# Kernel optimization log

Hardware: AMD Instinct MI355X
Metric: run time of the kernel (lower is better)

## Reference

```python
import jax, jax.numpy as jnp
import numpy as np

N_EMBD = 1024
N_HEAD = 16
HEAD = N_EMBD // N_HEAD


def setup_inputs() -> dict:
    key = jax.random.key(0)
    ks = jax.random.split(key, 5)
    B, T = 2, 2048
    s = 1.0 / np.sqrt(N_EMBD)
    return {
        "x": jax.random.normal(ks[0], (B, T, N_EMBD), jnp.float32),
        "w_attn": jax.random.normal(ks[1], (N_EMBD, 3 * N_EMBD), jnp.float32) * s,
        "b_attn": jnp.zeros((3 * N_EMBD,), jnp.float32),
        "w_proj": jax.random.normal(ks[2], (N_EMBD, N_EMBD), jnp.float32) * s,
        "b_proj": jnp.zeros((N_EMBD,), jnp.float32),
    }


def reference(x, w_attn, b_attn, w_proj, b_proj):
    B, T, C = x.shape
    qkv = x @ w_attn + b_attn                      # [B,T,3C]
    q, k, v = jnp.split(qkv, 3, axis=-1)
    def heads(t):
        return t.reshape(B, T, N_HEAD, HEAD).transpose(0, 2, 1, 3)  # [B,H,T,D]
    q, k, v = heads(q), heads(k), heads(v)
    scale = 1.0 / np.sqrt(HEAD)
    att = jnp.einsum('bhqd,bhkd->bhqk', q, k) * scale
    causal = jnp.tril(jnp.ones((T, T), bool))
    att = jnp.where(causal, att, -jnp.inf)
    p = jax.nn.softmax(att, axis=-1)
    y = jnp.einsum('bhqk,bhkd->bhqd', p, v)        # [B,H,T,D]
    y = y.transpose(0, 2, 1, 3).reshape(B, T, C)
    return y @ w_proj + b_proj
```

## Files before the change

### kernel.cpp

```cpp
#include <hip/hip_runtime.h>
#include <hip/hip_bf16.h>

typedef __attribute__((ext_vector_type(4))) float f32x4;
typedef __attribute__((ext_vector_type(16))) float f32x16;
typedef __attribute__((ext_vector_type(8))) short bf16x8;
typedef __attribute__((ext_vector_type(4))) unsigned int u32x4;

#define MFMA16(a,b,c) __builtin_amdgcn_mfma_f32_16x16x32_bf16(a,b,c,0,0,0)
#define MFMA32(a,b,c) __builtin_amdgcn_mfma_f32_32x32x16_bf16(a,b,c,0,0,0)
#define LOG2E 1.44269504088896340736f

__device__ __forceinline__ float bf2f(unsigned short u){
  unsigned v = ((unsigned)u) << 16;
  float f; __builtin_memcpy(&f, &v, 4); return f;
}
__device__ __forceinline__ unsigned short f2bf(float f){
  unsigned x; __builtin_memcpy(&x, &f, 4);
  x += 0x7fffu + ((x >> 16) & 1u);
  return (unsigned short)(x >> 16);
}
__device__ __forceinline__ void gload_lds16(const void* g, void* l){
  __builtin_amdgcn_global_load_lds((const __attribute__((address_space(1))) void*)g,
                                   (__attribute__((address_space(3))) void*)l, 16, 0, 0);
}
__device__ __forceinline__ f32x16 zero16(){
  f32x16 z;
#pragma unroll
  for (int i = 0; i < 16; ++i) z[i] = 0.f;
  return z;
}
__device__ __forceinline__ unsigned cvtpk(float lo, float hi_){
  unsigned d;
  asm("v_cvt_pk_bf16_f32 %0, %1, %2" : "=v"(d) : "v"(lo), "v"(hi_));
  return d;
}
__device__ __forceinline__ void pack_group(const float* p, bf16x8& f0, bf16x8& f1){
  unsigned a0 = cvtpk(p[0], p[1]),  b0 = cvtpk(p[4],  p[5]);
  unsigned a1 = cvtpk(p[2], p[3]),  b1 = cvtpk(p[6],  p[7]);
  unsigned c0 = cvtpk(p[8], p[9]),  d0 = cvtpk(p[12], p[13]);
  unsigned c1 = cvtpk(p[10],p[11]), d1 = cvtpk(p[14], p[15]);
  asm("v_permlane32_swap_b32 %0, %1" : "+v"(a0), "+v"(b0));
  asm("v_permlane32_swap_b32 %0, %1" : "+v"(a1), "+v"(b1));
  asm("v_permlane32_swap_b32 %0, %1" : "+v"(c0), "+v"(d0));
  asm("v_permlane32_swap_b32 %0, %1" : "+v"(c1), "+v"(d1));
  u32x4 w0 = {a0, a1, b0, b1};
  u32x4 w1 = {c0, c1, d0, d1};
  f0 = __builtin_bit_cast(bf16x8, w0);
  f1 = __builtin_bit_cast(bf16x8, w1);
}

__device__ __forceinline__ void castT_body(const float* __restrict__ src,
                                           unsigned short* __restrict__ dst,
                                           const int R, const int C,
                                           const int bx, const int by){
  __shared__ unsigned short t[64][65];
  const int r0 = by * 64, c0 = bx * 64;
  const int tid = threadIdx.x;
#pragma unroll
  for (int i = 0; i < 16; ++i){
    int idx = i*256 + tid; int r = idx >> 6, c = idx & 63;
    t[r][c] = f2bf(src[(size_t)(r0 + r)*C + c0 + c]);
  }
  __syncthreads();
#pragma unroll
  for (int i = 0; i < 16; ++i){
    int idx = i*256 + tid; int c = idx >> 6, r = idx & 63;
    dst[(size_t)(c0 + c)*R + r0 + r] = t[r][c];
  }
}
__global__ void k_prep(const float* __restrict__ wa, const float* __restrict__ wp,
                       unsigned short* __restrict__ waT, unsigned short* __restrict__ wpT){
  const int bx = blockIdx.x;
  if (bx < 48) castT_body(wa, waT, 1024, 3072, bx,      blockIdx.y);
  else         castT_body(wp, wpT, 1024, 1024, bx - 48, blockIdx.y);
}

__global__ __launch_bounds__(256,3) void k_gemm_qkv(const float* __restrict__ x,
    const unsigned short* __restrict__ waT, const float* __restrict__ b_attn,
    unsigned short* __restrict__ qb, unsigned short* __restrict__ kb,
    unsigned short* __restrict__ vb)
{
  __shared__ char lds[40960];
  const int K = 1024, NT = 32;
  const int tid = threadIdx.x, lane = tid & 63, wave = tid >> 6;
  const int wr = wave >> 1, wc = wave & 1;
  const int l15 = lane & 15, lg = lane >> 4;
  char* const ldsb = (char*)lds;

  f32x4 acc[4][4];
#pragma unroll
  for (int m = 0; m < 4; ++m)
#pragma unroll
    for (int n = 0; n < 4; ++n) acc[m][n] = (f32x4){0.f,0.f,0.f,0.f};

  const int hh0 = blockIdx.y * 24 + blockIdx.x;
  const int xcd = hh0 & 7, idx = hh0 >> 3;
  const int bm = (((xcd >> 1) << 3) + (idx & 7)) * 128;
  const int bn = ((xcd & 1) * 12 + (idx >> 3)) * 128;

  const int o = tid * 16;
  const int srow = o >> 6;
  const int sch = ((o >> 4) & 3) ^ ((srow >> 1) & 3);
  const float* gAf0 = x + (size_t)(bm + srow)*K      + sch*8;
  const float* gAf1 = x + (size_t)(bm + 64 + srow)*K + sch*8;
  const unsigned short* gB0 = waT + (size_t)(bn + srow)*K      + sch*8;
  const unsigned short* gB1 = waT + (size_t)(bn + 64 + srow)*K + sch*8;
  const int rsw = (l15 >> 1) & 3;
  const int aoff = (wr*64 + l15)*64 + ((lg ^ rsw) << 4);
  const int boff = (wc*64 + l15)*64 + ((lg ^ rsw) << 4);

  f32x4 aw[4];

#define ALOAD(T) do{ \
    aw[0] = *(const f32x4*)(gAf0 + (size_t)(T)*32); \
    aw[1] = *(const f32x4*)(gAf0 + (size_t)(T)*32 + 4); \
    aw[2] = *(const f32x4*)(gAf1 + (size_t)(T)*32); \
    aw[3] = *(const f32x4*)(gAf1 + (size_t)(T)*32 + 4); }while(0)
#define AWRITE(dstoff) do{ \
    u32x4 w0_ = { cvtpk(aw[0][0],aw[0][1]), cvtpk(aw[0][2],aw[0][3]), \
                  cvtpk(aw[1][0],aw[1][1]), cvtpk(aw[1][2],aw[1][3]) }; \
    u32x4 w1_ = { cvtpk(aw[2][0],aw[2][1]), cvtpk(aw[2][2],aw[2][3]), \
                  cvtpk(aw[3][0],aw[3][1]), cvtpk(aw[3][2],aw[3][3]) }; \
    *(u32x4*)(ldsb + (dstoff) + o) = w0_; \
    *(u32x4*)(ldsb + (dstoff) + 4096 + o) = w1_; }while(0)
#define BSTG(T, bb) do{ \
    gload_lds16(gB0 + (size_t)(T)*32, ldsb + 16384 + (bb) + o); \
    gload_lds16(gB1 + (size_t)(T)*32, ldsb + 16384 + (bb) + 4096 + o); }while(0)

  ALOAD(0);
  BSTG(0, 0);
  BSTG(1, 8192);
  asm volatile("s_waitcnt vmcnt(4)" ::: "memory");
  AWRITE(0);
  asm volatile("s_waitcnt vmcnt(2)" ::: "memory");
  asm volatile("s_waitcnt lgkmcnt(0)" ::: "memory");

  int abufc = 0;
  int bbufc = 0, bstg = 16384;
  for (int t = 0; t < NT; ++t){
    __builtin_amdgcn_s_barrier();
    __builtin_amdgcn_sched_barrier(0);
    if (t + 1 < NT) ALOAD(t + 1);
    if (t + 2 < NT) BSTG(t + 2, bstg);
    bf16x8 af[4], bg[4];
#pragma unroll
    for (int m = 0; m < 4; ++m) af[m] = *(const bf16x8*)(ldsb + abufc + aoff + m*1024);
#pragma unroll
    for (int n = 0; n < 4; ++n) bg[n] = *(const bf16x8*)(ldsb + 16384 + bbufc + boff + n*1024);
    __builtin_amdgcn_s_setprio(1);
#pragma unroll
    for (int m = 0; m < 4; ++m)
#pragma unroll
      for (int n = 0; n < 4; ++n)
        acc[m][n] = MFMA16(af[m], bg[n], acc[m][n]);
    __builtin_amdgcn_s_setprio(0);
    if (t + 2 < NT){
      asm volatile("s_waitcnt vmcnt(2)" ::: "memory");
      AWRITE(abufc ^ 8192);
    } else if (t + 1 < NT){
      asm volatile("s_waitcnt vmcnt(0)" ::: "memory");
      AWRITE(abufc ^ 8192);
    }
    asm volatile("s_waitcnt lgkmcnt(0)" ::: "memory");
    abufc ^= 8192;
    bbufc = (bbufc == 16384) ? 0 : bbufc + 8192;
    bstg  = (bstg  == 16384) ? 0 : bstg  + 8192;
  }
#undef ALOAD
#undef AWRITE
#undef BSTG

#pragma unroll
  for (int m = 0; m < 4; ++m){
#pragma unroll
    for (int n = 0; n < 4; ++n){
#pragma unroll
      for (int r = 0; r < 4; ++r){
        const int row = bm + wr*64 + m*16 + lg*4 + r;
        const int col = bn + wc*64 + n*16 + l15;
        const float val = acc[m][n][r] + b_attn[col];
        const int part = col >> 10, c = col & 1023;
        const int h = c >> 6, d = c & 63;
        const int b = row >> 11, t = row & 2047;
        const unsigned short u = f2bf(val);
        const size_t bhbase = (size_t)(b*16 + h)*131072;
        if (part == 0){
          qb[bhbase + (size_t)t*64 + d] = u;
        } else {
          const int tile = t >> 6, l = t & 63;
          const size_t base = bhbase + (size_t)tile*4096;
          if (part == 1) kb[base + l*64 + ((((d>>3)^(l&7))<<3) | (d&7))] = u;
          else           vb[base + d*64 + ((((l>>3)^(d&7))<<3) | (l&7))] = u;
        }
      }
    }
  }
}

__device__ __forceinline__ void gemm_core_s(const unsigned short* __restrict__ A,
                                            const unsigned short* __restrict__ Bt,
                                            const int K, const int bm, const int bn,
                                            char* ldsb, f32x4 acc[2][4])
{
  const int tid = threadIdx.x, lane = tid & 63, wave = tid >> 6;
  const int wr = wave >> 1, wc = wave & 1;
  const int l15 = lane & 15, lg = lane >> 4;
  const int o = tid * 16;
  const int srow = o >> 6;
  const int sch = ((o >> 4) & 3) ^ ((srow >> 1) & 3);
  const unsigned short* gA0 = A  + (size_t)(bm + srow)*K      + sch*8;
  const unsigned short* gB0 = Bt + (size_t)(bn + srow)*K      + sch*8;
  const unsigned short* gB1 = Bt + (size_t)(bn + 64 + srow)*K + sch*8;
  const int rsw = (l15 >> 1) & 3;
  const int aoff = (wr*32 + l15)*64 + ((lg ^ rsw) << 4);
  const int boff = 4096 + (wc*64 + l15)*64 + ((lg ^ rsw) << 4);

#define STGS(koff, bb) do { \
    gload_lds16(gA0 + (koff), ldsb + (bb) + o); \
    gload_lds16(gB0 + (koff), ldsb + (bb) + 4096 + o); \
    gload_lds16(gB1 + (koff), ldsb + (bb) + 8192 + o); } while(0)

  const int NT = K >> 5;
  STGS(0, 0);
  STGS(32, 12288);
  int bcur = 0, bstg = 24576;
  for (int t = 0; t < NT; ++t){
    if (t + 1 < NT) asm volatile("s_waitcnt vmcnt(3)" ::: "memory");
    else            asm volatile("s_waitcnt vmcnt(0)" ::: "memory");
    __builtin_amdgcn_s_barrier();
    __builtin_amdgcn_sched_barrier(0);
    if (t + 2 < NT) STGS((size_t)(t + 2) << 5, bstg);
    bf16x8 af[2], bg[4];
#pragma unroll
    for (int m = 0; m < 2; ++m) af[m] = *(const bf16x8*)(ldsb + bcur + aoff + m*1024);
#pragma unroll
    for (int n = 0; n < 4; ++n) bg[n] = *(const bf16x8*)(ldsb + bcur + boff + n*1024);
    __builtin_amdgcn_s_setprio(1);
#pragma unroll
    for (int m = 0; m < 2; ++m)
#pragma unroll
      for (int n = 0; n < 4; ++n)
        acc[m][n] = MFMA16(af[m], bg[n], acc[m][n]);
    __builtin_amdgcn_s_setprio(0);
    bcur = (bcur == 24576) ? 0 : bcur + 12288;
    bstg = (bstg == 24576) ? 0 : bstg + 12288;
  }
#undef STGS
}

__global__ __launch_bounds__(256,4) void k_gemm_proj(const unsigned short* __restrict__ yb,
    const unsigned short* __restrict__ wpT, const float* __restrict__ b_proj,
    float* __restrict__ out)
{
  __shared__ char lds[36864];
  f32x4 acc[2][4];
#pragma unroll
  for (int m = 0; m < 2; ++m)
#pragma unroll
    for (int n = 0; n < 4; ++n) acc[m][n] = (f32x4){0.f,0.f,0.f,0.f};
  int wgid = blockIdx.y * 8 + blockIdx.x;
  wgid = (wgid & 7) * 64 + (wgid >> 3);
  const int bm = (wgid / 8) * 64, bn = (wgid % 8) * 128;
  gemm_core_s(yb, wpT, 1024, bm, bn, lds, acc);
  const int lane = threadIdx.x & 63, wave = threadIdx.x >> 6;
  const int wr = wave >> 1, wc = wave & 1, l15 = lane & 15, lg = lane >> 4;
#pragma unroll
  for (int m = 0; m < 2; ++m){
#pragma unroll
    for (int n = 0; n < 4; ++n){
#pragma unroll
      for (int r = 0; r < 4; ++r){
        const int row = bm + wr*32 + m*16 + lg*4 + r;
        const int col = bn + wc*64 + n*16 + l15;
        out[(size_t)row*1024 + col] = acc[m][n][r] + b_proj[col];
      }
    }
  }
}

__global__ __launch_bounds__(256,2) void k_attn(const unsigned short* __restrict__ q,
                       const unsigned short* __restrict__ kt,
                       const unsigned short* __restrict__ vt,
                       unsigned short* __restrict__ y)
{
  __shared__ char lds[32768];
  const int tid = threadIdx.x, lane = tid & 63, wave = tid >> 6;
  const int l31 = lane & 31, hi = lane >> 5;
  const int i = blockIdx.x, ii = i & 255;
  const int bh = ii & 31;
  const int qbi = (i < 256) ? (15 - (ii >> 5)) : (ii >> 5);
  const int q0w = qbi*128 + wave*32;
  const int ntiles = (qbi + 1) * 2;
  const unsigned short* qh = q + (size_t)bh * 131072;
  const char* kbase = (const char*)(kt + (size_t)bh * 131072);
  const char* vbase = (const char*)(vt + (size_t)bh * 131072);

  const float C = 0.125f * LOG2E;
  const float M = 16.0f;

  bf16x8 qf[4];
  {
    const unsigned short* qp = qh + (size_t)(q0w + l31)*64 + hi*8;
#pragma unroll
    for (int ds = 0; ds < 4; ++ds) qf[ds] = *(const bf16x8*)(qp + ds*16);
  }

  f32x16 yac0 = zero16(), yac1 = zero16();
  float lsum = 0.f;
  const int mask_from = q0w >> 6;
  const int stg = tid * 16;
  const int dst = wave * 1024;
  char* ldsK = lds;
  char* ldsV = lds + 16384;

#define STAGE(tile, buf) do { \
    const char* ks_ = kbase + (size_t)(tile)*8192; \
    const char* vs_ = vbase + (size_t)(tile)*8192; \
    gload_lds16(ks_ + stg,        ldsK + (buf)*8192 + dst); \
    gload_lds16(ks_ + 4096 + stg, ldsK + (buf)*8192 + 4096 + dst); \
    gload_lds16(vs_ + stg,        ldsV + (buf)*8192 + dst); \
    gload_lds16(vs_ + 4096 + stg, ldsV + (buf)*8192 + 4096 + dst); \
  } while(0)

  STAGE(0, 0);
  __syncthreads();

  const int swz = (l31 & 7) << 4;
  const int rowb = l31 * 128;

  for (int t = 0; t < ntiles; ++t){
    const int buf = t & 1;
    if (t + 1 < ntiles) STAGE(t + 1, buf ^ 1);

    const char* kb_ = ldsK + buf*8192;
    const char* vb_ = ldsV + buf*8192;

    bf16x8 kf[8];
#pragma unroll
    for (int ds = 0; ds < 4; ++ds){
      const int ch = ((ds*2 + hi) << 4) ^ swz;
      kf[ds]   = *(const bf16x8*)(kb_ + rowb + ch);
      kf[ds+4] = *(const bf16x8*)(kb_ + 4096 + rowb + ch);
    }
    f32x16 s0 = zero16(), s1 = zero16();
#pragma unroll
    for (int ds = 0; ds < 4; ++ds){
      s0 = MFMA32(kf[ds],   qf[ds], s0);
      s1 = MFMA32(kf[ds+4], qf[ds], s1);
    }

    bf16x8 vf[8];
#pragma unroll
    for (int ks = 0; ks < 4; ++ks){
      const int ch = ((ks*2 + hi) << 4) ^ swz;
      vf[ks]   = *(const bf16x8*)(vb_ + rowb + ch);
      vf[ks+4] = *(const bf16x8*)(vb_ + 4096 + rowb + ch);
    }

    if (t >= mask_from){
      const int qg = q0w + l31, key0 = t << 6;
#pragma unroll
      for (int r = 0; r < 16; ++r){
        const int kl = (r&3) + 8*(r>>2) + 4*hi;
        if (key0 + kl      > qg) s0[r] = -1e30f;
        if (key0 + 32 + kl > qg) s1[r] = -1e30f;
      }
    }

    float p0[16], p1[16];
    float ts = 0.f;
#pragma unroll
    for (int r = 0; r < 16; ++r){
      p0[r] = __builtin_amdgcn_exp2f(__builtin_fmaf(s0[r], C, -M));
      p1[r] = __builtin_amdgcn_exp2f(__builtin_fmaf(s1[r], C, -M));
      ts += p0[r] + p1[r];
    }
    lsum += ts;

    bf16x8 pa[4];
    pack_group(p0, pa[0], pa[1]);
    pack_group(p1, pa[2], pa[3]);
#pragma unroll
    for (int ks = 0; ks < 4; ++ks){
      yac0 = MFMA32(pa[ks], vf[ks],   yac0);
      yac1 = MFMA32(pa[ks], vf[ks+4], yac1);
    }
    __syncthreads();
  }
#undef STAGE

  lsum += __shfl_xor(lsum, 32);
  const float linv = 1.0f / lsum;
  const int b = bh >> 4, h = bh & 15;
  unsigned short* yp = y + ((size_t)b*2048 + q0w)*1024 + h*64;
#pragma unroll
  for (int r = 0; r < 16; ++r){
    const int ql = (r&3) + 8*(r>>2) + 4*hi;
    const float li = __shfl(linv, ql);
    yp[(size_t)ql*1024 + l31]      = f2bf(yac0[r] * li);
    yp[(size_t)ql*1024 + 32 + l31] = f2bf(yac1[r] * li);
  }
}

extern "C" void kernel_launch(void* const* d_in, const int* in_sizes, int n_in,
                              void* d_out, int out_size, void* d_ws, size_t ws_size,
                              hipStream_t stream) {
  const float* x      = (const float*)d_in[0];
  const float* w_attn = (const float*)d_in[1];
  const float* b_attn = (const float*)d_in[2];
  const float* w_proj = (const float*)d_in[3];
  const float* b_proj = (const float*)d_in[4];
  float* out = (float*)d_out;

  unsigned short* ws  = (unsigned short*)d_ws;
  unsigned short* waT = ws;
  unsigned short* wpT = waT + 3145728;
  unsigned short* qb  = wpT + 1048576;
  unsigned short* kb  = qb  + 4194304;
  unsigned short* vb  = kb  + 4194304;
  unsigned short* yb  = vb  + 4194304;

  k_prep<<<dim3(64,16), dim3(256), 0, stream>>>(w_attn, w_proj, waT, wpT);
  k_gemm_qkv<<<dim3(24,32), dim3(256), 0, stream>>>(x, waT, b_attn, qb, kb, vb);
  k_attn<<<dim3(512), dim3(256), 0, stream>>>(qb, kb, vb, yb);
  k_gemm_proj<<<dim3(8,64), dim3(256), 0, stream>>>(yb, wpT, b_proj, out);
}
```

Before: 95.39 us.

## Deepen A-prefetch to two stages and compute softmax row sums via MFMA

In the QKV GEMM, the fp32 A-tile register prefetch is made two tiles deep with double-buffered registers, so global loads for A are issued alongside the B stage two iterations ahead and waits are relaxed. In attention, the per-lane exp sum and shuffle reduction are replaced by an extra MFMA against a vector of ones, which gives the row sums already laid out per output row. The denominator then comes from the bf16-rounded probabilities, matching what multiplies V. The cost is extra registers for the second A buffer and one extra MFMA per k-step, which may affect occupancy.

```diff
diff --git a/kernel.cpp b/kernel.cpp
--- a/kernel.cpp
+++ b/kernel.cpp
@@ -109,42 +109,41 @@
   const int aoff = (wr*64 + l15)*64 + ((lg ^ rsw) << 4);
   const int boff = (wc*64 + l15)*64 + ((lg ^ rsw) << 4);
 
-  f32x4 aw[4];
-
-#define ALOAD(T) do{ \
-    aw[0] = *(const f32x4*)(gAf0 + (size_t)(T)*32); \
-    aw[1] = *(const f32x4*)(gAf0 + (size_t)(T)*32 + 4); \
-    aw[2] = *(const f32x4*)(gAf1 + (size_t)(T)*32); \
-    aw[3] = *(const f32x4*)(gAf1 + (size_t)(T)*32 + 4); }while(0)
-#define AWRITE(dstoff) do{ \
-    u32x4 w0_ = { cvtpk(aw[0][0],aw[0][1]), cvtpk(aw[0][2],aw[0][3]), \
-                  cvtpk(aw[1][0],aw[1][1]), cvtpk(aw[1][2],aw[1][3]) }; \
-    u32x4 w1_ = { cvtpk(aw[2][0],aw[2][1]), cvtpk(aw[2][2],aw[2][3]), \
-                  cvtpk(aw[3][0],aw[3][1]), cvtpk(aw[3][2],aw[3][3]) }; \
+  f32x4 aw[2][4];
+
+#define ALOAD(T, S) do{ \
+    aw[S][0] = *(const f32x4*)(gAf0 + (size_t)(T)*32); \
+    aw[S][1] = *(const f32x4*)(gAf0 + (size_t)(T)*32 + 4); \
+    aw[S][2] = *(const f32x4*)(gAf1 + (size_t)(T)*32); \
+    aw[S][3] = *(const f32x4*)(gAf1 + (size_t)(T)*32 + 4); }while(0)
+#define AWRITE(S, dstoff) do{ \
+    u32x4 w0_ = { cvtpk(aw[S][0][0],aw[S][0][1]), cvtpk(aw[S][0][2],aw[S][0][3]), \
+                  cvtpk(aw[S][1][0],aw[S][1][1]), cvtpk(aw[S][1][2],aw[S][1][3]) }; \
+    u32x4 w1_ = { cvtpk(aw[S][2][0],aw[S][2][1]), cvtpk(aw[S][2][2],aw[S][2][3]), \
+                  cvtpk(aw[S][3][0],aw[S][3][1]), cvtpk(aw[S][3][2],aw[S][3][3]) }; \
     *(u32x4*)(ldsb + (dstoff) + o) = w0_; \
     *(u32x4*)(ldsb + (dstoff) + 4096 + o) = w1_; }while(0)
 #define BSTG(T, bb) do{ \
     gload_lds16(gB0 + (size_t)(T)*32, ldsb + 16384 + (bb) + o); \
     gload_lds16(gB1 + (size_t)(T)*32, ldsb + 16384 + (bb) + 4096 + o); }while(0)
 
-  ALOAD(0);
+  ALOAD(0, 0);
   BSTG(0, 0);
   BSTG(1, 8192);
-  asm volatile("s_waitcnt vmcnt(4)" ::: "memory");
-  AWRITE(0);
-  asm volatile("s_waitcnt vmcnt(2)" ::: "memory");
+  ALOAD(1, 1);
+  asm volatile("s_waitcnt vmcnt(8)" ::: "memory");
+  AWRITE(0, 0);
+  asm volatile("s_waitcnt vmcnt(6)" ::: "memory");
   asm volatile("s_waitcnt lgkmcnt(0)" ::: "memory");
 
-  int abufc = 0;
   int bbufc = 0, bstg = 16384;
   for (int t = 0; t < NT; ++t){
     __builtin_amdgcn_s_barrier();
     __builtin_amdgcn_sched_barrier(0);
-    if (t + 1 < NT) ALOAD(t + 1);
-    if (t + 2 < NT) BSTG(t + 2, bstg);
+    if (t + 2 < NT){ BSTG(t + 2, bstg); ALOAD(t + 2, t & 1); }
     bf16x8 af[4], bg[4];
 #pragma unroll
-    for (int m = 0; m < 4; ++m) af[m] = *(const bf16x8*)(ldsb + abufc + aoff + m*1024);
+    for (int m = 0; m < 4; ++m) af[m] = *(const bf16x8*)(ldsb + (t&1)*8192 + aoff + m*1024);
 #pragma unroll
     for (int n = 0; n < 4; ++n) bg[n] = *(const bf16x8*)(ldsb + 16384 + bbufc + boff + n*1024);
     __builtin_amdgcn_s_setprio(1);
@@ -154,15 +153,10 @@
       for (int n = 0; n < 4; ++n)
         acc[m][n] = MFMA16(af[m], bg[n], acc[m][n]);
     __builtin_amdgcn_s_setprio(0);
-    if (t + 2 < NT){
-      asm volatile("s_waitcnt vmcnt(2)" ::: "memory");
-      AWRITE(abufc ^ 8192);
-    } else if (t + 1 < NT){
-      asm volatile("s_waitcnt vmcnt(0)" ::: "memory");
-      AWRITE(abufc ^ 8192);
-    }
+    if (t + 2 < NT)      asm volatile("s_waitcnt vmcnt(6)" ::: "memory");
+    else if (t + 1 < NT) asm volatile("s_waitcnt vmcnt(0)" ::: "memory");
+    if (t + 1 < NT) AWRITE((t + 1) & 1, ((t + 1) & 1) * 8192);
     asm volatile("s_waitcnt lgkmcnt(0)" ::: "memory");
-    abufc ^= 8192;
     bbufc = (bbufc == 16384) ? 0 : bbufc + 8192;
     bstg  = (bstg  == 16384) ? 0 : bstg  + 8192;
   }
@@ -297,6 +291,7 @@
 
   const float C = 0.125f * LOG2E;
   const float M = 16.0f;
+  const bf16x8 ones = {0x3F80,0x3F80,0x3F80,0x3F80,0x3F80,0x3F80,0x3F80,0x3F80};
 
   bf16x8 qf[4];
   {
@@ -305,8 +300,7 @@
     for (int ds = 0; ds < 4; ++ds) qf[ds] = *(const bf16x8*)(qp + ds*16);
   }
 
-  f32x16 yac0 = zero16(), yac1 = zero16();
-  float lsum = 0.f;
+  f32x16 yac0 = zero16(), yac1 = zero16(), yacl = zero16();
   const int mask_from = q0w >> 6;
   const int stg = tid * 16;
   const int dst = wave * 1024;
@@ -368,14 +362,11 @@
     }
 
     float p0[16], p1[16];
-    float ts = 0.f;
 #pragma unroll
     for (int r = 0; r < 16; ++r){
       p0[r] = __builtin_amdgcn_exp2f(__builtin_fmaf(s0[r], C, -M));
       p1[r] = __builtin_amdgcn_exp2f(__builtin_fmaf(s1[r], C, -M));
-      ts += p0[r] + p1[r];
-    }
-    lsum += ts;
+    }
 
     bf16x8 pa[4];
     pack_group(p0, pa[0], pa[1]);
@@ -384,19 +375,18 @@
     for (int ks = 0; ks < 4; ++ks){
       yac0 = MFMA32(pa[ks], vf[ks],   yac0);
       yac1 = MFMA32(pa[ks], vf[ks+4], yac1);
+      yacl = MFMA32(pa[ks], ones,     yacl);
     }
     __syncthreads();
   }
 #undef STAGE
 
-  lsum += __shfl_xor(lsum, 32);
-  const float linv = 1.0f / lsum;
   const int b = bh >> 4, h = bh & 15;
   unsigned short* yp = y + ((size_t)b*2048 + q0w)*1024 + h*64;
 #pragma unroll
   for (int r = 0; r < 16; ++r){
     const int ql = (r&3) + 8*(r>>2) + 4*hi;
-    const float li = __shfl(linv, ql);
+    const float li = __builtin_amdgcn_rcpf(yacl[r]);
     yp[(size_t)ql*1024 + l31]      = f2bf(yac0[r] * li);
     yp[(size_t)ql*1024 + 32 + l31] = f2bf(yac1[r] * li);
   }
```

Result: slower. 105.9 us (+11.0%).
